# Optimization experiments

Measured on AMD Instinct MI355X. Metric: run time of the kernel, lower is better.

The kernel has to match this reference:

```python
import jax, jax.numpy as jnp
import numpy as np

B, S, D = 1, 2048, 2048
H, KV = 32, 8
HD = D // H          # 64
R = H // KV          # 4 (GQA repeat factor)
ROPE_BASE = 10000.0


def setup_inputs() -> dict:
    key = jax.random.key(0)
    ks = jax.random.split(key, 5)
    x = jax.random.normal(ks[0], (B, S, D), jnp.float32)
    # Real rotary frequencies as (cos, sin) pairs: [S, HD//2, 2]
    inv_freq = 1.0 / (ROPE_BASE ** (np.arange(0, HD, 2, dtype=np.float64) / HD))
    ang = np.outer(np.arange(S, dtype=np.float64), inv_freq)
    freqs_cis = jnp.asarray(np.stack([np.cos(ang), np.sin(ang)], axis=-1), jnp.float32)
    std = 0.02
    wq = jax.random.normal(ks[1], (H * HD, D), jnp.float32) * std
    wk = jax.random.normal(ks[2], (KV * HD, D), jnp.float32) * std
    wv = jax.random.normal(ks[3], (KV * HD, D), jnp.float32) * std
    wo = jax.random.normal(ks[4], (D, H * HD), jnp.float32) * std
    return {"x": x, "freqs_cis": freqs_cis, "wq": wq, "wk": wk, "wv": wv, "wo": wo}


def _apply_rope(x, cos, sin):
    # x: [b, s, h, hd]; cos/sin: [s, hd//2]. Complex multiply on interleaved pairs.
    xr = x.reshape(*x.shape[:-1], HD // 2, 2)
    x0, x1 = xr[..., 0], xr[..., 1]
    c = cos[None, :, None, :]
    s = sin[None, :, None, :]
    o0 = x0 * c - x1 * s
    o1 = x0 * s + x1 * c
    return jnp.stack([o0, o1], axis=-1).reshape(x.shape)


def reference(x, freqs_cis, wq, wk, wv, wo):
    b, s, _ = x.shape
    q = (x @ wq.T).reshape(b, s, H, HD)
    k = (x @ wk.T).reshape(b, s, KV, HD)
    v = (x @ wv.T).reshape(b, s, KV, HD)
    cos, sin = freqs_cis[..., 0], freqs_cis[..., 1]
    q = _apply_rope(q, cos, sin)
    k = _apply_rope(k, cos, sin)
    # GQA: group q heads instead of repeat_interleave on k/v.
    # repeat_interleave maps kv-head g -> q heads [g*R, (g+1)*R), matching this reshape.
    qg = q.reshape(b, s, KV, R, HD)
    scale = 1.0 / np.sqrt(HD)
    scores = jnp.einsum('bsgrd,btgd->bgrst', qg, k) * scale  # [b, KV, R, s, t]
    causal = jnp.tril(jnp.ones((s, s), dtype=bool))
    scores = jnp.where(causal, scores, jnp.float32(-1e9))
    attn = jax.nn.softmax(scores.astype(jnp.float32), axis=-1).astype(q.dtype)
    out = jnp.einsum('bgrst,btgd->bsgrd', attn, v).reshape(b, s, H * HD)
    return out @ wo.T
```

## Files before the change

### kernel.cpp

```cpp
#include <hip/hip_runtime.h>

typedef unsigned short u16;
typedef unsigned int u32;
typedef __bf16 bf16x8 __attribute__((ext_vector_type(8)));
typedef unsigned short ushort8 __attribute__((ext_vector_type(8)));
typedef float floatx4 __attribute__((ext_vector_type(4)));

#define S_LEN 2048
#define NH 32
#define NKV 8
#define HD_ 64
#define LDQ 3072

__device__ __forceinline__ u16 f2bf(float f) {
  unsigned u = __builtin_bit_cast(unsigned, f);
  u += 0x7FFF + ((u >> 16) & 1);
  return (u16)(u >> 16);
}
__device__ __forceinline__ float bf2f(u16 h) {
  unsigned u = ((unsigned)h) << 16;
  return __builtin_bit_cast(float, u);
}
__device__ __forceinline__ bf16x8 ld8(const u16* p) {
  return __builtin_bit_cast(bf16x8, *(const ushort8*)p);
}
__device__ __forceinline__ floatx4 mfma16(bf16x8 a, bf16x8 b, floatx4 c) {
  return __builtin_amdgcn_mfma_f32_16x16x32_bf16(a, b, c, 0, 0, 0);
}
__device__ __forceinline__ u32 pk2bf(float a, float b) {
  u32 ua = __builtin_bit_cast(u32, a) + 0x8000u;
  u32 ub = __builtin_bit_cast(u32, b) + 0x8000u;
  return __builtin_amdgcn_perm(ub, ua, 0x07060302);
}

__global__ void cvt_kernel(const float* __restrict__ in, u16* __restrict__ out, int n4) {
  int i = blockIdx.x * blockDim.x + threadIdx.x;
  if (i >= n4) return;
  float4 v = ((const float4*)in)[i];
  ((ushort4*)out)[i] = make_ushort4(f2bf(v.x), f2bf(v.y), f2bf(v.z), f2bf(v.w));
}

template <int TM, int TN, int OUT_BF16>
__global__ __launch_bounds__(256) void gemm_db(
    const u16* __restrict__ A, const u16* __restrict__ B, void* __restrict__ C,
    int ldc, int K, int lda) {
  __shared__ __align__(16) u16 As[2][TM * 64];
  __shared__ __align__(16) u16 Bs[2][TN * 64];
  const int tid = threadIdx.x;
  const int wave = tid >> 6, lane = tid & 63;
  const int quad = lane >> 4, l16 = lane & 15;
  const int bm = blockIdx.y * TM, bn = blockIdx.x * TN;
  const int wr = (wave >> 1) * (TM / 2), wc = (wave & 1) * (TN / 2);
  constexpr int MI = TM / 32, NI = TN / 32;
  const int crow = tid >> 3, col8 = tid & 7;

  size_t aoff[MI], boff[NI];
#pragma unroll
  for (int j = 0; j < MI; j++) aoff[j] = (size_t)(bm + crow + j * 32) * lda + col8 * 8;
#pragma unroll
  for (int j = 0; j < NI; j++) boff[j] = (size_t)(bn + crow + j * 32) * K + col8 * 8;

  ushort8 a8[MI], b8[NI];
  auto load_tiles = [&](int k0) {
#pragma unroll
    for (int j = 0; j < MI; j++) a8[j] = *(const ushort8*)(A + aoff[j] + k0);
#pragma unroll
    for (int j = 0; j < NI; j++) b8[j] = *(const ushort8*)(B + boff[j] + k0);
  };
  auto write_tiles = [&](int p) {
#pragma unroll
    for (int j = 0; j < MI; j++) {
      const int row = crow + j * 32;
      *(ushort8*)&As[p][row * 64 + ((col8 ^ (row & 7)) * 8)] = a8[j];
    }
#pragma unroll
    for (int j = 0; j < NI; j++) {
      const int row = crow + j * 32;
      *(ushort8*)&Bs[p][row * 64 + ((col8 ^ (row & 7)) * 8)] = b8[j];
    }
  };

  floatx4 acc[MI][NI] = {};
  load_tiles(0);
  write_tiles(0);
  __syncthreads();
  int p = 0;
  for (int k0 = 0; k0 < K; k0 += 64) {
    const bool more = (k0 + 64 < K);
    if (more) load_tiles(k0 + 64);
#pragma unroll
    for (int kh = 0; kh < 2; kh++) {
      bf16x8 af[MI], bfr[NI];
#pragma unroll
      for (int mi = 0; mi < MI; mi++) {
        const int row = wr + mi * 16 + l16;
        af[mi] = ld8(&As[p][row * 64 + (((kh * 4 + quad) ^ (row & 7)) * 8)]);
      }
#pragma unroll
      for (int ni = 0; ni < NI; ni++) {
        const int row = wc + ni * 16 + l16;
        bfr[ni] = ld8(&Bs[p][row * 64 + (((kh * 4 + quad) ^ (row & 7)) * 8)]);
      }
#pragma unroll
      for (int mi = 0; mi < MI; mi++)
#pragma unroll
        for (int ni = 0; ni < NI; ni++)
          acc[mi][ni] = mfma16(af[mi], bfr[ni], acc[mi][ni]);
    }
    if (more) {
      write_tiles(p ^ 1);
      __syncthreads();
      p ^= 1;
    }
  }

#pragma unroll
  for (int mi = 0; mi < MI; mi++)
#pragma unroll
    for (int ni = 0; ni < NI; ni++)
#pragma unroll
      for (int r = 0; r < 4; r++) {
        const int row = bm + wr + mi * 16 + quad * 4 + r;
        const int col = bn + wc + ni * 16 + l16;
        if (OUT_BF16) ((u16*)C)[(size_t)row * ldc + col] = f2bf(acc[mi][ni][r]);
        else          ((float*)C)[(size_t)row * ldc + col] = acc[mi][ni][r];
      }
}

__global__ void rope_kernel(u16* __restrict__ qk, const float* __restrict__ fc, int h_bits,
                            int row_stride, float scale) {
  int idx = blockIdx.x * blockDim.x + threadIdx.x;
  int d = idx & 31;
  int t = idx >> 5;
  int hh = t & ((1 << h_bits) - 1);
  int s = t >> h_bits;
  float c  = fc[s * 64 + d * 2];
  float sn = fc[s * 64 + d * 2 + 1];
  size_t base = (size_t)s * row_stride + hh * 64 + d * 2;
  float x0 = bf2f(qk[base]), x1 = bf2f(qk[base + 1]);
  qk[base]     = f2bf((x0 * c - x1 * sn) * scale);
  qk[base + 1] = f2bf((x0 * sn + x1 * c) * scale);
}

__global__ void transpose_v(const u16* __restrict__ qkv, u16* __restrict__ vT) {
  int idx = blockIdx.x * blockDim.x + threadIdx.x;
  int s = idx & (S_LEN - 1);
  int t = idx >> 11;
  vT[idx] = qkv[(size_t)s * LDQ + 2560 + t];
}

__global__ __launch_bounds__(256) void attn_kernel(const u16* qkv, const u16* __restrict__ vT,
                                                   u16* __restrict__ o) {
  __shared__ __align__(16) u16 Ks[64 * 72];
  __shared__ __align__(16) u16 Vs[64 * 72];
  __shared__ __align__(16) u16 pS[4][16 * 72];
  const int h = blockIdx.x;
  const int qt = (h & 1) ? (31 - (int)blockIdx.y) : (int)blockIdx.y;
  const int g = h >> 2;
  const int tid = threadIdx.x;
  const int wave = tid >> 6, lane = tid & 63;
  const int quad = lane >> 4, l16 = lane & 15;
  const int qglob = qt * 64 + wave * 16 + l16;

  const size_t qoff = (size_t)qglob * LDQ + h * HD_;
  bf16x8 qf0 = ld8(qkv + qoff + quad * 8);
  bf16x8 qf1 = ld8(qkv + qoff + 32 + quad * 8);

  const ushort8 ones_u = {0x3F80, 0x3F80, 0x3F80, 0x3F80, 0x3F80, 0x3F80, 0x3F80, 0x3F80};
  const bf16x8 onesA = __builtin_bit_cast(bf16x8, ones_u);

  const int r0 = tid >> 3,         o0 = (tid & 7) * 8;
  const int r1 = (tid + 256) >> 3, o1 = o0;
  const u16* ksrc = qkv + 2048 + g * HD_;
  const u16* vsrc = vT + (size_t)g * HD_ * S_LEN;

  ushort8 kp0 = *(const ushort8*)(ksrc + (size_t)r0 * LDQ + o0);
  ushort8 kp1 = *(const ushort8*)(ksrc + (size_t)r1 * LDQ + o1);
  ushort8 vp0 = *(const ushort8*)(vsrc + (size_t)r0 * S_LEN + o0);
  ushort8 vp1 = *(const ushort8*)(vsrc + (size_t)r1 * S_LEN + o1);

  floatx4 Ofrag[4] = {};
  floatx4 lacc = {};
  u16* myP = &pS[wave][0];

  for (int kt = 0; kt <= qt; kt++) {
    const int kbase = kt * 64;
    *(ushort8*)&Ks[r0 * 72 + o0] = kp0;
    *(ushort8*)&Ks[r1 * 72 + o1] = kp1;
    *(ushort8*)&Vs[r0 * 72 + o0] = vp0;
    *(ushort8*)&Vs[r1 * 72 + o1] = vp1;
    __syncthreads();
    if (kt < qt) {
      const int nb = kbase + 64;
      kp0 = *(const ushort8*)(ksrc + (size_t)(nb + r0) * LDQ + o0);
      kp1 = *(const ushort8*)(ksrc + (size_t)(nb + r1) * LDQ + o1);
      vp0 = *(const ushort8*)(vsrc + (size_t)r0 * S_LEN + nb + o0);
      vp1 = *(const ushort8*)(vsrc + (size_t)r1 * S_LEN + nb + o1);
    }
    floatx4 sf[4];
#pragma unroll
    for (int sub = 0; sub < 4; sub++) {
      const u16* kb = &Ks[(sub * 16 + l16) * 72];
      floatx4 s = {};
      s = mfma16(ld8(kb + quad * 8), qf0, s);
      s = mfma16(ld8(kb + 32 + quad * 8), qf1, s);
      sf[sub] = s;
    }
    if (kt == qt) {
#pragma unroll
      for (int sub = 0; sub < 4; sub++)
#pragma unroll
        for (int r = 0; r < 4; r++)
          if (kbase + sub * 16 + quad * 4 + r > qglob) sf[sub][r] = -INFINITY;
    }
    u32 pk[4][2];
#pragma unroll
    for (int sub = 0; sub < 4; sub++)
#pragma unroll
      for (int w = 0; w < 2; w++) {
        float p0 = __builtin_amdgcn_exp2f(sf[sub][2 * w]);
        float p1 = __builtin_amdgcn_exp2f(sf[sub][2 * w + 1]);
        pk[sub][w] = pk2bf(p0, p1);
      }
    bf16x8 vf[4][2];
#pragma unroll
    for (int nt = 0; nt < 4; nt++) {
      const u16* vb = &Vs[(nt * 16 + l16) * 72 + quad * 8];
      vf[nt][0] = ld8(vb);
      vf[nt][1] = ld8(vb + 32);
    }
#pragma unroll
    for (int sub = 0; sub < 4; sub++)
#pragma unroll
      for (int w = 0; w < 2; w++)
        *(u32*)&myP[l16 * 72 + sub * 16 + quad * 4 + 2 * w] = pk[sub][w];
    asm volatile("s_waitcnt lgkmcnt(0)" ::: "memory");
    bf16x8 pf0 = ld8(&myP[l16 * 72 + quad * 8]);
    bf16x8 pf1 = ld8(&myP[l16 * 72 + 32 + quad * 8]);
#pragma unroll
    for (int nt = 0; nt < 4; nt++) {
      Ofrag[nt] = mfma16(vf[nt][0], pf0, Ofrag[nt]);
      Ofrag[nt] = mfma16(vf[nt][1], pf1, Ofrag[nt]);
    }
    lacc = mfma16(onesA, pf0, lacc);
    lacc = mfma16(onesA, pf1, lacc);
    __syncthreads();
  }

  const float inv = 1.0f / lacc[0];
  const size_t ooff = (size_t)qglob * 2048 + h * HD_;
#pragma unroll
  for (int nt = 0; nt < 4; nt++)
#pragma unroll
    for (int r = 0; r < 4; r++) {
      int hd = nt * 16 + quad * 4 + r;
      o[ooff + hd] = f2bf(Ofrag[nt][r] * inv);
    }
}

extern "C" void kernel_launch(void* const* d_in, const int* in_sizes, int n_in,
                              void* d_out, int out_size, void* d_ws, size_t ws_size,
                              hipStream_t stream) {
  const float* x  = (const float*)d_in[0];
  const float* fc = (const float*)d_in[1];
  const float* wq = (const float*)d_in[2];
  const float* wk = (const float*)d_in[3];
  const float* wv = (const float*)d_in[4];
  const float* wo = (const float*)d_in[5];
  float* out = (float*)d_out;

  char* ws = (char*)d_ws;
  const size_t MB = 1024 * 1024;
  u16* qkv = (u16*)(ws);
  u16* wb  = (u16*)(ws + 12 * MB);
  u16* vTb = (u16*)(ws + 12 * MB);
  u16* wob = (u16*)(ws + 14 * MB);
  u16* ob  = (u16*)(ws + 22 * MB);
  u16* xb  = (u16*)d_out;
  (void)ws_size; (void)n_in; (void)in_sizes; (void)out_size;

  cvt_kernel<<<4096, 256, 0, stream>>>(x,  xb, 1048576);
  cvt_kernel<<<4096, 256, 0, stream>>>(wq, wb, 1048576);
  cvt_kernel<<<1024, 256, 0, stream>>>(wk, wb + (size_t)2048 * 2048, 262144);
  cvt_kernel<<<1024, 256, 0, stream>>>(wv, wb + (size_t)2560 * 2048, 262144);
  gemm_db<128, 96, 1><<<dim3(32, 16), 256, 0, stream>>>(xb, wb, qkv, LDQ, 2048, 2048);
  cvt_kernel<<<4096, 256, 0, stream>>>(wo, wob, 1048576);
  rope_kernel<<<8192, 256, 0, stream>>>(qkv, fc, 5, LDQ, 0.18033688f);
  rope_kernel<<<2048, 256, 0, stream>>>(qkv + 2048, fc, 3, LDQ, 1.0f);
  transpose_v<<<4096, 256, 0, stream>>>(qkv, vTb);
  attn_kernel<<<dim3(NH, S_LEN / 64), 256, 0, stream>>>(qkv, vTb, ob);
  gemm_db<128, 64, 0><<<dim3(32, 16), 256, 0, stream>>>(ob, wob, out, 2048, 2048, 2048);
}
```

Measured before the change: 236.2 us.

## Pair causal query tiles per attention block for balanced work

Result: no change. 233.8 us (-1.0%).

```diff
diff --git a/kernel.cpp b/kernel.cpp
--- a/kernel.cpp
+++ b/kernel.cpp
@@ -5,6 +5,7 @@
 typedef __bf16 bf16x8 __attribute__((ext_vector_type(8)));
 typedef unsigned short ushort8 __attribute__((ext_vector_type(8)));
 typedef float floatx4 __attribute__((ext_vector_type(4)));
+typedef u32 u32x2 __attribute__((ext_vector_type(2)));
 
 #define S_LEN 2048
 #define NH 32
@@ -155,19 +156,23 @@
   __shared__ __align__(16) u16 Vs[64 * 72];
   __shared__ __align__(16) u16 pS[4][16 * 72];
   const int h = blockIdx.x;
-  const int qt = (h & 1) ? (31 - (int)blockIdx.y) : (int)blockIdx.y;
   const int g = h >> 2;
   const int tid = threadIdx.x;
   const int wave = tid >> 6, lane = tid & 63;
   const int quad = lane >> 4, l16 = lane & 15;
-  const int qglob = qt * 64 + wave * 16 + l16;
-
-  const size_t qoff = (size_t)qglob * LDQ + h * HD_;
-  bf16x8 qf0 = ld8(qkv + qoff + quad * 8);
-  bf16x8 qf1 = ld8(qkv + qoff + 32 + quad * 8);
+  const int qtA = (int)blockIdx.y;
+  const int qtB = 31 - qtA;
 
   const ushort8 ones_u = {0x3F80, 0x3F80, 0x3F80, 0x3F80, 0x3F80, 0x3F80, 0x3F80, 0x3F80};
   const bf16x8 onesA = __builtin_bit_cast(bf16x8, ones_u);
+
+  const int qrow = wave * 16 + l16;
+  const size_t qoffA = (size_t)(qtA * 64 + qrow) * LDQ + h * HD_;
+  const size_t qoffB = (size_t)(qtB * 64 + qrow) * LDQ + h * HD_;
+  bf16x8 qfA0 = ld8(qkv + qoffA + quad * 8);
+  bf16x8 qfA1 = ld8(qkv + qoffA + 32 + quad * 8);
+  bf16x8 qfB0 = ld8(qkv + qoffB + quad * 8);
+  bf16x8 qfB1 = ld8(qkv + qoffB + 32 + quad * 8);
 
   const int r0 = tid >> 3,         o0 = (tid & 7) * 8;
   const int r1 = (tid + 256) >> 3, o1 = o0;
@@ -179,83 +184,90 @@
   ushort8 vp0 = *(const ushort8*)(vsrc + (size_t)r0 * S_LEN + o0);
   ushort8 vp1 = *(const ushort8*)(vsrc + (size_t)r1 * S_LEN + o1);
 
-  floatx4 Ofrag[4] = {};
-  floatx4 lacc = {};
   u16* myP = &pS[wave][0];
 
-  for (int kt = 0; kt <= qt; kt++) {
-    const int kbase = kt * 64;
-    *(ushort8*)&Ks[r0 * 72 + o0] = kp0;
-    *(ushort8*)&Ks[r1 * 72 + o1] = kp1;
-    *(ushort8*)&Vs[r0 * 72 + o0] = vp0;
-    *(ushort8*)&Vs[r1 * 72 + o1] = vp1;
-    __syncthreads();
-    if (kt < qt) {
-      const int nb = kbase + 64;
-      kp0 = *(const ushort8*)(ksrc + (size_t)(nb + r0) * LDQ + o0);
-      kp1 = *(const ushort8*)(ksrc + (size_t)(nb + r1) * LDQ + o1);
-      vp0 = *(const ushort8*)(vsrc + (size_t)r0 * S_LEN + nb + o0);
-      vp1 = *(const ushort8*)(vsrc + (size_t)r1 * S_LEN + nb + o1);
-    }
-    floatx4 sf[4];
-#pragma unroll
-    for (int sub = 0; sub < 4; sub++) {
-      const u16* kb = &Ks[(sub * 16 + l16) * 72];
-      floatx4 s = {};
-      s = mfma16(ld8(kb + quad * 8), qf0, s);
-      s = mfma16(ld8(kb + 32 + quad * 8), qf1, s);
-      sf[sub] = s;
-    }
-    if (kt == qt) {
+  for (int ph = 0; ph < 2; ph++) {
+    const int qt = ph ? qtB : qtA;
+    const int qglob = qt * 64 + qrow;
+    const bf16x8 qf0 = ph ? qfB0 : qfA0;
+    const bf16x8 qf1 = ph ? qfB1 : qfA1;
+    floatx4 Ofrag[4] = {};
+    floatx4 lacc = {};
+
+    for (int kt = 0; kt <= qt; kt++) {
+      const int kbase = kt * 64;
+      *(ushort8*)&Ks[r0 * 72 + o0] = kp0;
+      *(ushort8*)&Ks[r1 * 72 + o1] = kp1;
+      *(ushort8*)&Vs[r0 * 72 + o0] = vp0;
+      *(ushort8*)&Vs[r1 * 72 + o1] = vp1;
+      __syncthreads();
+      const bool last = (kt == qt);
+      if (!last || ph == 0) {
+        const int nb = last ? 0 : kbase + 64;
+        kp0 = *(const ushort8*)(ksrc + (size_t)(nb + r0) * LDQ + o0);
+        kp1 = *(const ushort8*)(ksrc + (size_t)(nb + r1) * LDQ + o1);
+        vp0 = *(const ushort8*)(vsrc + (size_t)r0 * S_LEN + nb + o0);
+        vp1 = *(const ushort8*)(vsrc + (size_t)r1 * S_LEN + nb + o1);
+      }
+      floatx4 sf[4];
+#pragma unroll
+      for (int sub = 0; sub < 4; sub++) {
+        const u16* kb = &Ks[(sub * 16 + l16) * 72];
+        floatx4 s = {};
+        s = mfma16(ld8(kb + quad * 8), qf0, s);
+        s = mfma16(ld8(kb + 32 + quad * 8), qf1, s);
+        sf[sub] = s;
+      }
+      if (last) {
+#pragma unroll
+        for (int sub = 0; sub < 4; sub++)
+#pragma unroll
+          for (int r = 0; r < 4; r++)
+            if (kbase + sub * 16 + quad * 4 + r > qglob) sf[sub][r] = -INFINITY;
+      }
+      u32x2 pk[4];
+#pragma unroll
+      for (int sub = 0; sub < 4; sub++) {
+        float p0 = __builtin_amdgcn_exp2f(sf[sub][0]);
+        float p1 = __builtin_amdgcn_exp2f(sf[sub][1]);
+        float p2 = __builtin_amdgcn_exp2f(sf[sub][2]);
+        float p3 = __builtin_amdgcn_exp2f(sf[sub][3]);
+        pk[sub].x = pk2bf(p0, p1);
+        pk[sub].y = pk2bf(p2, p3);
+      }
+      bf16x8 vf[4][2];
+#pragma unroll
+      for (int nt = 0; nt < 4; nt++) {
+        const u16* vb = &Vs[(nt * 16 + l16) * 72 + quad * 8];
+        vf[nt][0] = ld8(vb);
+        vf[nt][1] = ld8(vb + 32);
+      }
 #pragma unroll
       for (int sub = 0; sub < 4; sub++)
-#pragma unroll
-        for (int r = 0; r < 4; r++)
-          if (kbase + sub * 16 + quad * 4 + r > qglob) sf[sub][r] = -INFINITY;
-    }
-    u32 pk[4][2];
-#pragma unroll
-    for (int sub = 0; sub < 4; sub++)
-#pragma unroll
-      for (int w = 0; w < 2; w++) {
-        float p0 = __builtin_amdgcn_exp2f(sf[sub][2 * w]);
-        float p1 = __builtin_amdgcn_exp2f(sf[sub][2 * w + 1]);
-        pk[sub][w] = pk2bf(p0, p1);
-      }
-    bf16x8 vf[4][2];
-#pragma unroll
-    for (int nt = 0; nt < 4; nt++) {
-      const u16* vb = &Vs[(nt * 16 + l16) * 72 + quad * 8];
-      vf[nt][0] = ld8(vb);
-      vf[nt][1] = ld8(vb + 32);
-    }
-#pragma unroll
-    for (int sub = 0; sub < 4; sub++)
-#pragma unroll
-      for (int w = 0; w < 2; w++)
-        *(u32*)&myP[l16 * 72 + sub * 16 + quad * 4 + 2 * w] = pk[sub][w];
-    asm volatile("s_waitcnt lgkmcnt(0)" ::: "memory");
-    bf16x8 pf0 = ld8(&myP[l16 * 72 + quad * 8]);
-    bf16x8 pf1 = ld8(&myP[l16 * 72 + 32 + quad * 8]);
-#pragma unroll
-    for (int nt = 0; nt < 4; nt++) {
-      Ofrag[nt] = mfma16(vf[nt][0], pf0, Ofrag[nt]);
-      Ofrag[nt] = mfma16(vf[nt][1], pf1, Ofrag[nt]);
-    }
-    lacc = mfma16(onesA, pf0, lacc);
-    lacc = mfma16(onesA, pf1, lacc);
-    __syncthreads();
+        *(u32x2*)&myP[l16 * 72 + sub * 16 + quad * 4] = pk[sub];
+      asm volatile("s_waitcnt lgkmcnt(0)" ::: "memory");
+      bf16x8 pf0 = ld8(&myP[l16 * 72 + quad * 8]);
+      bf16x8 pf1 = ld8(&myP[l16 * 72 + 32 + quad * 8]);
+#pragma unroll
+      for (int nt = 0; nt < 4; nt++) {
+        Ofrag[nt] = mfma16(vf[nt][0], pf0, Ofrag[nt]);
+        Ofrag[nt] = mfma16(vf[nt][1], pf1, Ofrag[nt]);
+      }
+      lacc = mfma16(onesA, pf0, lacc);
+      lacc = mfma16(onesA, pf1, lacc);
+      __syncthreads();
+    }
+
+    const float inv = 1.0f / lacc[0];
+    const size_t ooff = (size_t)qglob * 2048 + h * HD_;
+#pragma unroll
+    for (int nt = 0; nt < 4; nt++)
+#pragma unroll
+      for (int r = 0; r < 4; r++) {
+        int hd = nt * 16 + quad * 4 + r;
+        o[ooff + hd] = f2bf(Ofrag[nt][r] * inv);
+      }
   }
-
-  const float inv = 1.0f / lacc[0];
-  const size_t ooff = (size_t)qglob * 2048 + h * HD_;
-#pragma unroll
-  for (int nt = 0; nt < 4; nt++)
-#pragma unroll
-    for (int r = 0; r < 4; r++) {
-      int hd = nt * 16 + quad * 4 + r;
-      o[ooff + hd] = f2bf(Ofrag[nt][r] * inv);
-    }
 }
 
 extern "C" void kernel_launch(void* const* d_in, const int* in_sizes, int n_in,
@@ -288,6 +300,6 @@
   rope_kernel<<<8192, 256, 0, stream>>>(qkv, fc, 5, LDQ, 0.18033688f);
   rope_kernel<<<2048, 256, 0, stream>>>(qkv + 2048, fc, 3, LDQ, 1.0f);
   transpose_v<<<4096, 256, 0, stream>>>(qkv, vTb);
-  attn_kernel<<<dim3(NH, S_LEN / 64), 256, 0, stream>>>(qkv, vTb, ob);
+  attn_kernel<<<dim3(NH, 16), 256, 0, stream>>>(qkv, vTb, ob);
   gemm_db<128, 64, 0><<<dim3(32, 16), 256, 0, stream>>>(ob, wob, out, 2048, 2048, 2048);
 }
```
